# Kernel optimization log

Hardware: AMD Instinct MI355X
Metric: run time of the kernel (lower is better)

## Reference

```python
import jax, jax.numpy as jnp
import numpy as np

NEG = -1e30  # finite stand-in for -inf (keeps grads NaN-free)

T, B, V, L = 1024, 64, 128, 256


def setup_inputs() -> dict:
    key = jax.random.key(0)
    k1, k2 = jax.random.split(key)
    acts = jax.random.normal(k1, (T, B, V), dtype=jnp.float32)
    # flat concatenated labels, values in [1, V) (0 is the blank)
    labels = jax.random.randint(k2, (B * L,), 1, V, dtype=jnp.int32)
    act_lens = jnp.full((B,), T, dtype=jnp.int32)
    label_lens = jnp.full((B,), L, dtype=jnp.int32)
    return {"acts": acts, "labels": labels, "act_lens": act_lens, "label_lens": label_lens}


def _ctc_costs(acts, labels, act_lens, label_lens):
    # warp-ctc takes raw activations and applies softmax internally
    Tt, Bb, Vv = acts.shape
    Ll = labels.shape[0] // Bb
    blank = 0
    lab = labels.reshape(Bb, Ll)
    S = 2 * Ll + 1
    # extended label seq: blank, l1, blank, l2, ..., blank  -> (B, S)
    ext = jnp.full((Bb, S), blank, dtype=labels.dtype).at[:, 1::2].set(lab)
    # skip transition allowed where ext[s] != blank and ext[s] != ext[s-2]
    allow = jnp.concatenate(
        [jnp.zeros((Bb, 2), dtype=bool), (ext[:, 2:] != blank) & (ext[:, 2:] != ext[:, :-2])],
        axis=1,
    )
    log_probs = jax.nn.log_softmax(acts, axis=-1)  # (T, B, V)
    # emission log-probs along the extended label sequence: (T, B, S)
    emit_all = jnp.take_along_axis(log_probs, jnp.broadcast_to(ext[None], (Tt, Bb, S)), axis=2)

    alpha0 = (
        jnp.full((Bb, S), NEG, dtype=acts.dtype)
        .at[:, 0].set(emit_all[0, :, 0])
        .at[:, 1].set(emit_all[0, :, 1])
    )

    def step(alpha, xs):
        emit, t = xs  # emit: (B, S)
        p1 = jnp.pad(alpha[:, :-1], ((0, 0), (1, 0)), constant_values=NEG)
        p2 = jnp.pad(alpha[:, :-2], ((0, 0), (2, 0)), constant_values=NEG)
        p2 = jnp.where(allow, p2, NEG)
        m = jnp.maximum(jnp.maximum(alpha, p1), p2)
        new = m + jnp.log(jnp.exp(alpha - m) + jnp.exp(p1 - m) + jnp.exp(p2 - m)) + emit
        # freeze rows whose act_len is exhausted
        alpha = jnp.where((t < act_lens)[:, None], new, alpha)
        return alpha, None

    alphaT, _ = jax.lax.scan(step, alpha0, (emit_all[1:], jnp.arange(1, Tt)))
    end = (2 * label_lens).astype(jnp.int32)  # last blank position per example
    a_end = jnp.take_along_axis(alphaT, end[:, None], axis=1)[:, 0]
    a_end1 = jnp.take_along_axis(alphaT, (end - 1)[:, None], axis=1)[:, 0]
    return -jnp.logaddexp(a_end, a_end1)  # per-example negative log-likelihood


def reference(acts, labels, act_lens, label_lens):
    costs = _ctc_costs(acts, labels, act_lens, label_lens)
    return jnp.sum(costs)  # reduce=True, no size/length averaging
```

## Files before the change

### kernel.cpp

```cpp
#include <hip/hip_runtime.h>
#include <hip/hip_fp16.h>
#include <math.h>


#define L2E 1.4426950408889634f
#define LN2 0.6931471805599453f

constexpr int T   = 1024;
constexpr int B   = 64;
constexpr int V   = 128;
constexpr int L   = 256;
constexpr int RW  = 256;
constexpr int TP  = T + 32;

typedef float v2f __attribute__((ext_vector_type(2)));
typedef unsigned int v2u __attribute__((ext_vector_type(2)));

__device__ __forceinline__ v2f pk_fma(v2f a, v2f b, v2f c) {
  v2f d; asm("v_pk_fma_f32 %0, %1, %2, %3" : "=v"(d) : "v"(a), "v"(b), "v"(c));
  return d;
}
__device__ __forceinline__ v2f pk_mul(v2f a, v2f b) {
  v2f d; asm("v_pk_mul_f32 %0, %1, %2" : "=v"(d) : "v"(a), "v"(b)); return d;
}
__device__ __forceinline__ v2f pk_mul_s(v2f a, v2f sb) {
  v2f d; asm("v_pk_mul_f32 %0, %1, %2" : "=v"(d) : "v"(a), "s"(sb)); return d;
}
__device__ __forceinline__ v2f pk_fma_s(v2f a, v2f sb, v2f c) {
  v2f d; asm("v_pk_fma_f32 %0, %1, %2, %3" : "=v"(d) : "v"(a), "s"(sb), "v"(c));
  return d;
}

template <int CTRL>
__device__ __forceinline__ float fdpp0(float x) {
  return __int_as_float(__builtin_amdgcn_update_dpp(
      0, __float_as_int(x), CTRL, 0xf, 0xf, true));
}
template <int CTRL>
__device__ __forceinline__ float fdppk(float x) {
  return __int_as_float(__builtin_amdgcn_update_dpp(
      __float_as_int(x), __float_as_int(x), CTRL, 0xf, 0xf, false));
}

__device__ __forceinline__ float wave_bcast63(float x) {
  return __int_as_float(__builtin_amdgcn_readlane(__float_as_int(x), 63));
}

__device__ __forceinline__ float wave_max(float x) {
  x = fmaxf(x, fdppk<0x111>(x));
  x = fmaxf(x, fdppk<0x112>(x));
  x = fmaxf(x, fdppk<0x114>(x));
  x = fmaxf(x, fdppk<0x118>(x));
  x = fmaxf(x, fdppk<0x142>(x));
  x = fmaxf(x, fdppk<0x143>(x));
  return wave_bcast63(x);
}
__device__ __forceinline__ float wave_sum_nn(float x) {
  x += fdpp0<0x111>(x);
  x += fdpp0<0x112>(x);
  x += fdpp0<0x114>(x);
  x += fdpp0<0x118>(x);
  x += fdpp0<0x142>(x);
  x += fdpp0<0x143>(x);
  return wave_bcast63(x);
}

__device__ __forceinline__ float h2f(uint bits) {
  return __half2float(__ushort_as_half((ushort)bits));
}

__global__ __launch_bounds__(256) void ctc_probs_kernel(
    const float* __restrict__ acts,
    const int* __restrict__ labels,
    ushort* __restrict__ P,
    float* __restrict__ Pbk) {
  const int w    = threadIdx.x >> 6;
  const int lane = threadIdx.x & 63;
  const int b    = blockIdx.y;
  const int tb   = blockIdx.x * 32 + w * 8;

  if (tb >= T) {
    #pragma unroll
    for (int r = 0; r < 8; ++r) {
      uint2 z; z.x = 0u; z.y = 0u;
      *(uint2*)(P + ((size_t)b * TP + tb + r) * RW + 4 * lane) = z;
    }
    if (lane < 8) {
      v2f zp; zp.x = 0.f; zp.y = 0.f;
      *(v2f*)(Pbk + ((size_t)b * TP + tb + lane) * 2) = zp;
    }
    return;
  }

  const int4 lvv = *(const int4*)(labels + (size_t)b * L + 4 * lane);
  const int ba0 = (lvv.x & ~1) * 2, sh0 = (lvv.x & 1) << 4;
  const int ba1 = (lvv.y & ~1) * 2, sh1 = (lvv.y & 1) << 4;
  const int ba2 = (lvv.z & ~1) * 2, sh2 = (lvv.z & 1) << 4;
  const int ba3 = (lvv.w & ~1) * 2, sh3 = (lvv.w & 1) << 4;

  #pragma unroll
  for (int r = 0; r < 8; ++r) {
    const int t = tb + r;
    const float* row = acts + ((size_t)t * B + b) * V;
    const float2 v2 = *(const float2*)(row + 2 * lane);
    const float e0 = exp2f(fmaf(v2.x, L2E, -32.0f));
    const float e1 = exp2f(fmaf(v2.y, L2E, -32.0f));
    const float sm = wave_sum_nn(e0 + e1);
    const float rc = __builtin_amdgcn_rcpf(sm);
    const auto pk = __builtin_amdgcn_cvt_pkrtz(e0 * rc, e1 * rc);
    uint hp;
    __builtin_memcpy(&hp, &pk, 4);
    const uint g0 = (uint)__builtin_amdgcn_ds_bpermute(ba0, (int)hp);
    const uint g1 = (uint)__builtin_amdgcn_ds_bpermute(ba1, (int)hp);
    const uint g2 = (uint)__builtin_amdgcn_ds_bpermute(ba2, (int)hp);
    const uint g3 = (uint)__builtin_amdgcn_ds_bpermute(ba3, (int)hp);
    const uint h0 = (g0 >> sh0) & 0xffffu;
    const uint h1 = (g1 >> sh1) & 0xffffu;
    const uint h2 = (g2 >> sh2);
    const uint h3 = (g3 >> sh3);
    uint2 o;
    o.x = h0 | (h2 << 16);
    o.y = h1 | (h3 << 16);
    *(uint2*)(P + ((size_t)b * TP + t) * RW + 4 * lane) = o;
    if (lane == 0) {
      const float pb = e0 * rc;
      v2f bp; bp.x = pb; bp.y = pb;
      *(v2f*)(Pbk + ((size_t)b * TP + t) * 2) = bp;
    }
  }
}

__global__ __launch_bounds__(64) void ctc_dp_kernel(
    const ushort* __restrict__ P,
    const float* __restrict__ Pbk,
    const int* __restrict__ labels,
    const int* __restrict__ act_lens,
    const int* __restrict__ label_lens,
    float* __restrict__ out) {
  const int b    = blockIdx.x;
  const int lane = threadIdx.x;
  const ushort* __restrict__ Pb = P + (size_t)b * TP * RW;
  const float*  __restrict__ Bk = Pbk + (size_t)b * TP * 2;

  const int4 lv   = *(const int4*)(labels + (size_t)b * L + 4 * lane);
  const int prevw = __builtin_amdgcn_update_dpp(0, lv.w, 0x138, 0xf, 0xf, true);
  const float f0 = (lane > 0 && lv.x != 0 && lv.x != prevw) ? 1.f : 0.f;
  const float f1 = (lv.y != 0 && lv.y != lv.x) ? 1.f : 0.f;
  const float f2 = (lv.z != 0 && lv.z != lv.y) ? 1.f : 0.f;
  const float f3 = (lv.w != 0 && lv.w != lv.z) ? 1.f : 0.f;
  v2f F02; F02.x = f0; F02.y = f2;
  v2f F13; F13.x = f1; F13.y = f3;

  const int AL = act_lens[b];

  v2f P0, P1, P2, P3;
  P0.x=0.f; P0.y=0.f; P1.x=0.f; P1.y=0.f;
  P2.x=0.f; P2.y=0.f; P3.x=0.f; P3.y=0.f;
  float a8 = 0.f;
  {
    const uint2 u0 = *(const uint2*)(Pb + 4 * lane);
    const v2f bk0  = *(const v2f*)(Bk);
    const float eb0 = bk0.x;
    const float e00 = h2f(u0.x);
    if (lane == 0) { P0.x = eb0; P1.x = e00; }
  }
  int iacc = 0;
  float pend = 1.0f;

  auto step = [&](v2u u, v2f eb) {
    const float pc = fdpp0<0x138>(P3.y);
    v2f Q; Q.x = pc; Q.y = P3.x;
    v2f E02, E13;
    E02.x = h2f(u.x); E02.y = h2f(u.x >> 16);
    E13.x = h2f(u.y); E13.y = h2f(u.y >> 16);
    const v2f A1 = pk_fma(F02, Q, P0);
    const v2f A3 = pk_fma(F13, P1, P2);
    const v2f ZQ = pk_mul_s(Q, eb);
    const v2f Z2 = pk_mul_s(P1, eb);
    const v2f Z1 = pk_mul(A1, E02);
    const v2f Z3 = pk_mul(A3, E13);
    const float z8 = P3.y * eb.x;
    P0 = pk_fma_s(P0, eb, ZQ);
    P1 = pk_fma(P1, E02, Z1);
    P2 = pk_fma_s(P2, eb, Z2);
    P3 = pk_fma(P3, E13, Z3);
    a8 = fmaf(a8, eb.x, z8);
  };

  auto measure = [&]() {
    float m = fmaxf(fmaxf(fmaxf(P0.x, P0.y), fmaxf(P1.x, P1.y)),
                    fmaxf(fmaxf(P2.x, P2.y), fmaxf(P3.x, P3.y)));
    m = fmaxf(m, a8);
    pend = wave_max(m);
  };
  auto apply = [&]() {
    const uint mb = __float_as_uint(pend);
    int e = (int)((mb >> 23) & 0xffu); if (e < 48) e = 48;
    const float r = __uint_as_float((uint)(302 - e) << 23);
    iacc += (e - 175);
    v2f rr; rr.x = r; rr.y = r;
    P0 = pk_mul(P0, rr); P1 = pk_mul(P1, rr);
    P2 = pk_mul(P2, rr); P3 = pk_mul(P3, rr);
    a8 *= r;
  };

  uint2 evi[16];
  #pragma unroll
  for (int k = 0; k < 16; ++k)
    evi[k] = *(const uint2*)(Pb + (size_t)(1 + k) * RW + 4 * lane);
  v2f ebq[16];
  #pragma unroll
  for (int k = 0; k < 16; ++k)
    ebq[k] = *(const v2f*)(Bk + (size_t)(1 + k) * 2);

  const ushort* pf = Pb + (size_t)17 * RW;
  int t0 = 1;
  #pragma unroll 1
  for (int blk = 0; blk < 64; ++blk) {
    v2f ebn[16];
    {
      const float* bn = Bk + (size_t)(t0 + 16) * 2;
      #pragma unroll
      for (int k = 0; k < 16; ++k) ebn[k] = *(const v2f*)(bn + 2 * k);
    }
    const ushort* pfA = pf;
    const ushort* pfB = pf + (size_t)8 * RW;
    const bool fast = (t0 + 16 <= AL);
    if (fast) {
      #pragma unroll
      for (int k = 0; k < 16; ++k) {
        const uint2 uu = evi[k];
        v2u u; u.x = uu.x; u.y = uu.y;
        evi[k] = *(const uint2*)(((k < 8) ? pfA : pfB)
                                 + (size_t)(k & 7) * RW + 4 * lane);
        step(u, ebq[k]);
        if (k == 13) measure();
        if (k == 15) apply();
      }
    } else {
      #pragma unroll
      for (int k = 0; k < 16; ++k) {
        const uint2 uu = evi[k];
        v2u u; u.x = uu.x; u.y = uu.y;
        evi[k] = *(const uint2*)(((k < 8) ? pfA : pfB)
                                 + (size_t)(k & 7) * RW + 4 * lane);
        if ((t0 + k) < AL) step(u, ebq[k]);
        if (k == 13) measure();
        if (k == 15) apply();
      }
    }
    #pragma unroll
    for (int k = 0; k < 16; ++k) ebq[k] = ebn[k];
    t0 += 16;
    pf += (size_t)16 * RW;
  }

  const int end  = 2 * label_lens[b];
  const int base = 8 * lane;
  float sel = 0.f;
  if (base     == end || base     == end - 1) sel += P0.x;
  if (base + 1 == end || base + 1 == end - 1) sel += P1.x;
  if (base + 2 == end || base + 2 == end - 1) sel += P2.x;
  if (base + 3 == end || base + 3 == end - 1) sel += P3.x;
  if (base + 4 == end || base + 4 == end - 1) sel += P0.y;
  if (base + 5 == end || base + 5 == end - 1) sel += P1.y;
  if (base + 6 == end || base + 6 == end - 1) sel += P2.y;
  if (base + 7 == end || base + 7 == end - 1) sel += P3.y;
  if (lane == 63 && (end == 512 || end - 1 == 512)) sel += a8;
  sel = wave_sum_nn(sel);
  if (lane == 0) {
    const float cost = -((log2f(sel) + (float)iacc) * LN2);
    atomicAdd(out, cost);
  }
}

extern "C" void kernel_launch(void* const* d_in, const int* in_sizes, int n_in,
                              void* d_out, int out_size, void* d_ws, size_t ws_size,
                              hipStream_t stream) {
  const float* acts       = (const float*)d_in[0];
  const int*   labels     = (const int*)d_in[1];
  const int*   act_lens   = (const int*)d_in[2];
  const int*   label_lens = (const int*)d_in[3];
  float* out = (float*)d_out;
  ushort* P   = (ushort*)d_ws;
  float*  Pbk = (float*)(P + (size_t)B * TP * RW);

  (void)hipMemsetAsync(out, 0, sizeof(float) * out_size, stream);
  ctc_probs_kernel<<<dim3(TP / 32, B), 256, 0, stream>>>(acts, labels, P, Pbk);
  ctc_dp_kernel<<<B, 64, 0, stream>>>(P, Pbk, labels, act_lens, label_lens, out);
}
```

Baseline: 150.2 us.

## Split CTC alpha recursion across eight waves with overlapping halo lanes

The DP kernel moves from one wave per example, where each lane held 8 states, to 512 threads (8 waves) per example, with each lane holding 2 states. Waves overlap by 32 lanes as a halo, so each wave advances 16 timesteps on its own, then trades boundary state through shared memory and a block barrier. The scale max also becomes block-wide through shared memory. The probs kernel changes its fp16 packing order and stores the blank probability once instead of duplicated. This is meant to shorten the serial dependency chain per step, at the cost of redundant halo compute, a __syncthreads every 16 steps, and halo accuracy that relies on the 32-lane overlap covering 16 steps of propagation.

```diff
diff --git a/kernel.cpp b/kernel.cpp
--- a/kernel.cpp
+++ b/kernel.cpp
@@ -14,22 +14,6 @@
 constexpr int TP  = T + 32;
 
 typedef float v2f __attribute__((ext_vector_type(2)));
-typedef unsigned int v2u __attribute__((ext_vector_type(2)));
-
-__device__ __forceinline__ v2f pk_fma(v2f a, v2f b, v2f c) {
-  v2f d; asm("v_pk_fma_f32 %0, %1, %2, %3" : "=v"(d) : "v"(a), "v"(b), "v"(c));
-  return d;
-}
-__device__ __forceinline__ v2f pk_mul(v2f a, v2f b) {
-  v2f d; asm("v_pk_mul_f32 %0, %1, %2" : "=v"(d) : "v"(a), "v"(b)); return d;
-}
-__device__ __forceinline__ v2f pk_mul_s(v2f a, v2f sb) {
-  v2f d; asm("v_pk_mul_f32 %0, %1, %2" : "=v"(d) : "v"(a), "s"(sb)); return d;
-}
-__device__ __forceinline__ v2f pk_fma_s(v2f a, v2f sb, v2f c) {
-  v2f d; asm("v_pk_fma_f32 %0, %1, %2, %3" : "=v"(d) : "v"(a), "s"(sb), "v"(c));
-  return d;
-}
 
 template <int CTRL>
 __device__ __forceinline__ float fdpp0(float x) {
@@ -85,10 +69,7 @@
       uint2 z; z.x = 0u; z.y = 0u;
       *(uint2*)(P + ((size_t)b * TP + tb + r) * RW + 4 * lane) = z;
     }
-    if (lane < 8) {
-      v2f zp; zp.x = 0.f; zp.y = 0.f;
-      *(v2f*)(Pbk + ((size_t)b * TP + tb + lane) * 2) = zp;
-    }
+    if (lane < 8) Pbk[(size_t)b * TP + tb + lane] = 0.f;
     return;
   }
 
@@ -116,160 +97,158 @@
     const uint g3 = (uint)__builtin_amdgcn_ds_bpermute(ba3, (int)hp);
     const uint h0 = (g0 >> sh0) & 0xffffu;
     const uint h1 = (g1 >> sh1) & 0xffffu;
-    const uint h2 = (g2 >> sh2);
+    const uint h2 = (g2 >> sh2) & 0xffffu;
     const uint h3 = (g3 >> sh3);
     uint2 o;
-    o.x = h0 | (h2 << 16);
-    o.y = h1 | (h3 << 16);
+    o.x = h0 | (h1 << 16);
+    o.y = h2 | (h3 << 16);
     *(uint2*)(P + ((size_t)b * TP + t) * RW + 4 * lane) = o;
-    if (lane == 0) {
-      const float pb = e0 * rc;
-      v2f bp; bp.x = pb; bp.y = pb;
-      *(v2f*)(Pbk + ((size_t)b * TP + t) * 2) = bp;
-    }
-  }
-}
-
-__global__ __launch_bounds__(64) void ctc_dp_kernel(
+    if (lane == 0)
+      Pbk[(size_t)b * TP + t] = e0 * rc;
+  }
+}
+
+__global__ __launch_bounds__(512) void ctc_dp_kernel(
     const ushort* __restrict__ P,
     const float* __restrict__ Pbk,
     const int* __restrict__ labels,
     const int* __restrict__ act_lens,
     const int* __restrict__ label_lens,
     float* __restrict__ out) {
+  __shared__ float shc[2][9 * 64];
+  __shared__ float shm[2][8];
+  __shared__ float shs[8];
   const int b    = blockIdx.x;
-  const int lane = threadIdx.x;
+  const int w    = threadIdx.x >> 6;
+  const int lane = threadIdx.x & 63;
+  const int k    = 32 * w - 32 + lane;
+  const int kc   = (k < 0) ? 0 : k;
   const ushort* __restrict__ Pb = P + (size_t)b * TP * RW;
-  const float*  __restrict__ Bk = Pbk + (size_t)b * TP * 2;
-
-  const int4 lv   = *(const int4*)(labels + (size_t)b * L + 4 * lane);
-  const int prevw = __builtin_amdgcn_update_dpp(0, lv.w, 0x138, 0xf, 0xf, true);
-  const float f0 = (lane > 0 && lv.x != 0 && lv.x != prevw) ? 1.f : 0.f;
-  const float f1 = (lv.y != 0 && lv.y != lv.x) ? 1.f : 0.f;
-  const float f2 = (lv.z != 0 && lv.z != lv.y) ? 1.f : 0.f;
-  const float f3 = (lv.w != 0 && lv.w != lv.z) ? 1.f : 0.f;
-  v2f F02; F02.x = f0; F02.y = f2;
-  v2f F13; F13.x = f1; F13.y = f3;
+  const float*  __restrict__ Bk = Pbk + (size_t)b * TP;
+
+  if (threadIdx.x < 64) {
+    shc[0][threadIdx.x] = 0.f;
+    shc[1][threadIdx.x] = 0.f;
+  }
+
+  float f = 0.f;
+  if (k >= 1) {
+    const int la  = labels[(size_t)b * L + k];
+    const int lam = labels[(size_t)b * L + k - 1];
+    f = (la != 0 && la != lam) ? 1.f : 0.f;
+  }
 
   const int AL = act_lens[b];
-
-  v2f P0, P1, P2, P3;
-  P0.x=0.f; P0.y=0.f; P1.x=0.f; P1.y=0.f;
-  P2.x=0.f; P2.y=0.f; P3.x=0.f; P3.y=0.f;
+  const ushort* __restrict__ PbL = Pb + kc;
+
+  v2f Pp; Pp.x = 0.f; Pp.y = 0.f;
   float a8 = 0.f;
   {
-    const uint2 u0 = *(const uint2*)(Pb + 4 * lane);
-    const v2f bk0  = *(const v2f*)(Bk);
-    const float eb0 = bk0.x;
-    const float e00 = h2f(u0.x);
-    if (lane == 0) { P0.x = eb0; P1.x = e00; }
+    const float eb0 = Bk[0];
+    const float e00 = h2f(PbL[0]);
+    if (k == 0) { Pp.x = eb0; Pp.y = e00; }
   }
   int iacc = 0;
-  float pend = 1.0f;
-
-  auto step = [&](v2u u, v2f eb) {
-    const float pc = fdpp0<0x138>(P3.y);
-    v2f Q; Q.x = pc; Q.y = P3.x;
-    v2f E02, E13;
-    E02.x = h2f(u.x); E02.y = h2f(u.x >> 16);
-    E13.x = h2f(u.y); E13.y = h2f(u.y >> 16);
-    const v2f A1 = pk_fma(F02, Q, P0);
-    const v2f A3 = pk_fma(F13, P1, P2);
-    const v2f ZQ = pk_mul_s(Q, eb);
-    const v2f Z2 = pk_mul_s(P1, eb);
-    const v2f Z1 = pk_mul(A1, E02);
-    const v2f Z3 = pk_mul(A3, E13);
-    const float z8 = P3.y * eb.x;
-    P0 = pk_fma_s(P0, eb, ZQ);
-    P1 = pk_fma(P1, E02, Z1);
-    P2 = pk_fma_s(P2, eb, Z2);
-    P3 = pk_fma(P3, E13, Z3);
-    a8 = fmaf(a8, eb.x, z8);
-  };
-
-  auto measure = [&]() {
-    float m = fmaxf(fmaxf(fmaxf(P0.x, P0.y), fmaxf(P1.x, P1.y)),
-                    fmaxf(fmaxf(P2.x, P2.y), fmaxf(P3.x, P3.y)));
-    m = fmaxf(m, a8);
-    pend = wave_max(m);
-  };
-  auto apply = [&]() {
-    const uint mb = __float_as_uint(pend);
-    int e = (int)((mb >> 23) & 0xffu); if (e < 48) e = 48;
-    const float r = __uint_as_float((uint)(302 - e) << 23);
-    iacc += (e - 175);
-    v2f rr; rr.x = r; rr.y = r;
-    P0 = pk_mul(P0, rr); P1 = pk_mul(P1, rr);
-    P2 = pk_mul(P2, rr); P3 = pk_mul(P3, rr);
-    a8 *= r;
-  };
-
-  uint2 evi[16];
+
+  uint ev[16];
   #pragma unroll
-  for (int k = 0; k < 16; ++k)
-    evi[k] = *(const uint2*)(Pb + (size_t)(1 + k) * RW + 4 * lane);
-  v2f ebq[16];
+  for (int j = 0; j < 16; ++j) ev[j] = PbL[(size_t)(1 + j) * RW];
+  float bkq[16];
   #pragma unroll
-  for (int k = 0; k < 16; ++k)
-    ebq[k] = *(const v2f*)(Bk + (size_t)(1 + k) * 2);
-
-  const ushort* pf = Pb + (size_t)17 * RW;
+  for (int j = 0; j < 16; ++j) bkq[j] = Bk[1 + j];
+
+  const ushort* pf = PbL + (size_t)17 * RW;
   int t0 = 1;
   #pragma unroll 1
   for (int blk = 0; blk < 64; ++blk) {
-    v2f ebn[16];
+    const int bb = blk & 1;
+    float bkn[16];
     {
-      const float* bn = Bk + (size_t)(t0 + 16) * 2;
+      const float* bn = Bk + (t0 + 16);
       #pragma unroll
-      for (int k = 0; k < 16; ++k) ebn[k] = *(const v2f*)(bn + 2 * k);
+      for (int j = 0; j < 16; ++j) bkn[j] = bn[j];
     }
     const ushort* pfA = pf;
     const ushort* pfB = pf + (size_t)8 * RW;
     const bool fast = (t0 + 16 <= AL);
     if (fast) {
       #pragma unroll
-      for (int k = 0; k < 16; ++k) {
-        const uint2 uu = evi[k];
-        v2u u; u.x = uu.x; u.y = uu.y;
-        evi[k] = *(const uint2*)(((k < 8) ? pfA : pfB)
-                                 + (size_t)(k & 7) * RW + 4 * lane);
-        step(u, ebq[k]);
-        if (k == 13) measure();
-        if (k == 15) apply();
+      for (int kk = 0; kk < 16; ++kk) {
+        const uint uu = ev[kk];
+        ev[kk] = ((kk < 8) ? pfA : pfB)[(size_t)(kk & 7) * RW];
+        const float pc = fdpp0<0x138>(Pp.y);
+        const float e  = h2f(uu);
+        const float sx = Pp.x + pc;
+        const float ty = fmaf(f, pc, Pp.y + Pp.x);
+        const float s8 = a8 + Pp.y;
+        Pp.x = sx * bkq[kk];
+        Pp.y = ty * e;
+        a8 = s8 * bkq[kk];
+        if (kk == 13) {
+          const float m = fmaxf(fmaxf(Pp.x, Pp.y), a8);
+          const float pm = wave_max(m);
+          if (lane == 0) shm[bb][w] = pm;
+        }
       }
     } else {
       #pragma unroll
-      for (int k = 0; k < 16; ++k) {
-        const uint2 uu = evi[k];
-        v2u u; u.x = uu.x; u.y = uu.y;
-        evi[k] = *(const uint2*)(((k < 8) ? pfA : pfB)
-                                 + (size_t)(k & 7) * RW + 4 * lane);
-        if ((t0 + k) < AL) step(u, ebq[k]);
-        if (k == 13) measure();
-        if (k == 15) apply();
+      for (int kk = 0; kk < 16; ++kk) {
+        const uint uu = ev[kk];
+        ev[kk] = ((kk < 8) ? pfA : pfB)[(size_t)(kk & 7) * RW];
+        if ((t0 + kk) < AL) {
+          const float pc = fdpp0<0x138>(Pp.y);
+          const float e  = h2f(uu);
+          const float sx = Pp.x + pc;
+          const float ty = fmaf(f, pc, Pp.y + Pp.x);
+          const float s8 = a8 + Pp.y;
+          Pp.x = sx * bkq[kk];
+          Pp.y = ty * e;
+          a8 = s8 * bkq[kk];
+        }
+        if (kk == 13) {
+          const float m = fmaxf(fmaxf(Pp.x, Pp.y), a8);
+          const float pm = wave_max(m);
+          if (lane == 0) shm[bb][w] = pm;
+        }
       }
     }
+    if (lane >= 32)
+      *(v2f*)&shc[bb][(w + 1) * 64 + 2 * (lane - 32)] = Pp;
+    __syncthreads();
+    const float* mm = shm[bb];
+    const float bm = fmaxf(fmaxf(fmaxf(mm[0], mm[1]), fmaxf(mm[2], mm[3])),
+                           fmaxf(fmaxf(mm[4], mm[5]), fmaxf(mm[6], mm[7])));
+    if (lane < 32)
+      Pp = *(const v2f*)&shc[bb][w * 64 + 2 * lane];
+    {
+      const uint mb2 = __float_as_uint(bm);
+      int e = (int)((mb2 >> 23) & 0xffu); if (e < 48) e = 48;
+      const float r = __uint_as_float((uint)(302 - e) << 23);
+      iacc += (e - 175);
+      Pp.x *= r; Pp.y *= r; a8 *= r;
+    }
     #pragma unroll
-    for (int k = 0; k < 16; ++k) ebq[k] = ebn[k];
+    for (int j = 0; j < 16; ++j) bkq[j] = bkn[j];
     t0 += 16;
     pf += (size_t)16 * RW;
   }
 
-  const int end  = 2 * label_lens[b];
-  const int base = 8 * lane;
+  const int end = 2 * label_lens[b];
   float sel = 0.f;
-  if (base     == end || base     == end - 1) sel += P0.x;
-  if (base + 1 == end || base + 1 == end - 1) sel += P1.x;
-  if (base + 2 == end || base + 2 == end - 1) sel += P2.x;
-  if (base + 3 == end || base + 3 == end - 1) sel += P3.x;
-  if (base + 4 == end || base + 4 == end - 1) sel += P0.y;
-  if (base + 5 == end || base + 5 == end - 1) sel += P1.y;
-  if (base + 6 == end || base + 6 == end - 1) sel += P2.y;
-  if (base + 7 == end || base + 7 == end - 1) sel += P3.y;
-  if (lane == 63 && (end == 512 || end - 1 == 512)) sel += a8;
+  if (lane >= 32) {
+    const int c0 = 64 * w + 2 * (lane - 32);
+    if (c0 == end || c0 == end - 1) sel += Pp.x;
+    if (c0 + 1 == end || c0 + 1 == end - 1) sel += Pp.y;
+  }
+  if (w == 7 && lane == 63 && end == 512) sel += a8;
   sel = wave_sum_nn(sel);
-  if (lane == 0) {
-    const float cost = -((log2f(sel) + (float)iacc) * LN2);
+  if (lane == 0) shs[w] = sel;
+  __syncthreads();
+  if (threadIdx.x == 0) {
+    float s = 0.f;
+    #pragma unroll
+    for (int j = 0; j < 8; ++j) s += shs[j];
+    const float cost = -((log2f(s) + (float)iacc) * LN2);
     atomicAdd(out, cost);
   }
 }
@@ -287,5 +266,5 @@
 
   (void)hipMemsetAsync(out, 0, sizeof(float) * out_size, stream);
   ctc_probs_kernel<<<dim3(TP / 32, B), 256, 0, stream>>>(acts, labels, P, Pbk);
-  ctc_dp_kernel<<<B, 64, 0, stream>>>(P, Pbk, labels, act_lens, label_lens, out);
-}
+  ctc_dp_kernel<<<B, 512, 0, stream>>>(P, Pbk, labels, act_lens, label_lens, out);
+}
```

Result: faster. 142.9 us (-4.9%).

## Replace packed-FP32 DP step with scalar add-then-multiply inline asm

Applied to the files above, without the earlier changes.

The CTC alpha recurrence step moves from packed v_pk_fma/v_pk_mul on interleaved register pairs to a scalar form: add neighbours, fmac the skip term, then multiply by the emission, written as one hand-scheduled inline-asm block. The probability layout is changed to a natural contiguous half order, and the blank-probability buffer is stored as single floats instead of duplicated pairs, with its loads interleaved into the prefetch loop. The aim is a shorter serial dependency chain per timestep and fewer registers for prefetch buffers, at the cost of giving up packed throughput and fixing the schedule in asm volatile.

```diff
diff --git a/kernel.cpp b/kernel.cpp
--- a/kernel.cpp
+++ b/kernel.cpp
@@ -12,24 +12,6 @@
 constexpr int L   = 256;
 constexpr int RW  = 256;
 constexpr int TP  = T + 32;
-
-typedef float v2f __attribute__((ext_vector_type(2)));
-typedef unsigned int v2u __attribute__((ext_vector_type(2)));
-
-__device__ __forceinline__ v2f pk_fma(v2f a, v2f b, v2f c) {
-  v2f d; asm("v_pk_fma_f32 %0, %1, %2, %3" : "=v"(d) : "v"(a), "v"(b), "v"(c));
-  return d;
-}
-__device__ __forceinline__ v2f pk_mul(v2f a, v2f b) {
-  v2f d; asm("v_pk_mul_f32 %0, %1, %2" : "=v"(d) : "v"(a), "v"(b)); return d;
-}
-__device__ __forceinline__ v2f pk_mul_s(v2f a, v2f sb) {
-  v2f d; asm("v_pk_mul_f32 %0, %1, %2" : "=v"(d) : "v"(a), "s"(sb)); return d;
-}
-__device__ __forceinline__ v2f pk_fma_s(v2f a, v2f sb, v2f c) {
-  v2f d; asm("v_pk_fma_f32 %0, %1, %2, %3" : "=v"(d) : "v"(a), "s"(sb), "v"(c));
-  return d;
-}
 
 template <int CTRL>
 __device__ __forceinline__ float fdpp0(float x) {
@@ -67,6 +49,46 @@
 
 __device__ __forceinline__ float h2f(uint bits) {
   return __half2float(__ushort_as_half((ushort)bits));
+}
+
+__device__ __forceinline__ void step22(
+    float& a0, float& a1, float& a2, float& a3, float& a4,
+    float& a5, float& a6, float& a7, float& a8,
+    float pc, float e0, float e1, float e2, float e3, float eb,
+    float f0, float f1, float f2, float f3) {
+  float s0, s1, s2, s3, s4, s5, s6, s7, s8;
+  asm volatile(
+      "v_add_f32 %[s8], %[x8], %[x7]\n\t"
+      "v_add_f32 %[s7], %[x7], %[x6]\n\t"
+      "v_add_f32 %[s6], %[x6], %[x5]\n\t"
+      "v_add_f32 %[s5], %[x5], %[x4]\n\t"
+      "v_add_f32 %[s4], %[x4], %[x3]\n\t"
+      "v_add_f32 %[s3], %[x3], %[x2]\n\t"
+      "v_add_f32 %[s2], %[x2], %[x1]\n\t"
+      "v_add_f32 %[s1], %[x1], %[x0]\n\t"
+      "v_add_f32 %[s0], %[x0], %[pc]\n\t"
+      "v_fmac_f32 %[s7], %[f3], %[x5]\n\t"
+      "v_fmac_f32 %[s5], %[f2], %[x3]\n\t"
+      "v_fmac_f32 %[s3], %[f1], %[x1]\n\t"
+      "v_fmac_f32 %[s1], %[f0], %[pc]\n\t"
+      "v_mul_f32 %[x8], %[s8], %[eb]\n\t"
+      "v_mul_f32 %[x7], %[s7], %[e3]\n\t"
+      "v_mul_f32 %[x6], %[s6], %[eb]\n\t"
+      "v_mul_f32 %[x5], %[s5], %[e2]\n\t"
+      "v_mul_f32 %[x4], %[s4], %[eb]\n\t"
+      "v_mul_f32 %[x3], %[s3], %[e1]\n\t"
+      "v_mul_f32 %[x2], %[s2], %[eb]\n\t"
+      "v_mul_f32 %[x1], %[s1], %[e0]\n\t"
+      "v_mul_f32 %[x0], %[s0], %[eb]\n\t"
+      : [s0] "=&v"(s0), [s1] "=&v"(s1), [s2] "=&v"(s2), [s3] "=&v"(s3),
+        [s4] "=&v"(s4), [s5] "=&v"(s5), [s6] "=&v"(s6), [s7] "=&v"(s7),
+        [s8] "=&v"(s8),
+        [x0] "+v"(a0), [x1] "+v"(a1), [x2] "+v"(a2), [x3] "+v"(a3),
+        [x4] "+v"(a4), [x5] "+v"(a5), [x6] "+v"(a6), [x7] "+v"(a7),
+        [x8] "+v"(a8)
+      : [pc] "v"(pc), [e0] "v"(e0), [e1] "v"(e1), [e2] "v"(e2),
+        [e3] "v"(e3), [eb] "v"(eb), [f0] "v"(f0), [f1] "v"(f1),
+        [f2] "v"(f2), [f3] "v"(f3));
 }
 
 __global__ __launch_bounds__(256) void ctc_probs_kernel(
@@ -85,10 +107,7 @@
       uint2 z; z.x = 0u; z.y = 0u;
       *(uint2*)(P + ((size_t)b * TP + tb + r) * RW + 4 * lane) = z;
     }
-    if (lane < 8) {
-      v2f zp; zp.x = 0.f; zp.y = 0.f;
-      *(v2f*)(Pbk + ((size_t)b * TP + tb + lane) * 2) = zp;
-    }
+    if (lane < 8) Pbk[(size_t)b * TP + tb + lane] = 0.f;
     return;
   }
 
@@ -116,17 +135,14 @@
     const uint g3 = (uint)__builtin_amdgcn_ds_bpermute(ba3, (int)hp);
     const uint h0 = (g0 >> sh0) & 0xffffu;
     const uint h1 = (g1 >> sh1) & 0xffffu;
-    const uint h2 = (g2 >> sh2);
+    const uint h2 = (g2 >> sh2) & 0xffffu;
     const uint h3 = (g3 >> sh3);
     uint2 o;
-    o.x = h0 | (h2 << 16);
-    o.y = h1 | (h3 << 16);
+    o.x = h0 | (h1 << 16);
+    o.y = h2 | (h3 << 16);
     *(uint2*)(P + ((size_t)b * TP + t) * RW + 4 * lane) = o;
-    if (lane == 0) {
-      const float pb = e0 * rc;
-      v2f bp; bp.x = pb; bp.y = pb;
-      *(v2f*)(Pbk + ((size_t)b * TP + t) * 2) = bp;
-    }
+    if (lane == 0)
+      Pbk[(size_t)b * TP + t] = e0 * rc;
   }
 }
 
@@ -140,7 +156,7 @@
   const int b    = blockIdx.x;
   const int lane = threadIdx.x;
   const ushort* __restrict__ Pb = P + (size_t)b * TP * RW;
-  const float*  __restrict__ Bk = Pbk + (size_t)b * TP * 2;
+  const float*  __restrict__ Bk = Pbk + (size_t)b * TP;
 
   const int4 lv   = *(const int4*)(labels + (size_t)b * L + 4 * lane);
   const int prevw = __builtin_amdgcn_update_dpp(0, lv.w, 0x138, 0xf, 0xf, true);
@@ -148,48 +164,22 @@
   const float f1 = (lv.y != 0 && lv.y != lv.x) ? 1.f : 0.f;
   const float f2 = (lv.z != 0 && lv.z != lv.y) ? 1.f : 0.f;
   const float f3 = (lv.w != 0 && lv.w != lv.z) ? 1.f : 0.f;
-  v2f F02; F02.x = f0; F02.y = f2;
-  v2f F13; F13.x = f1; F13.y = f3;
 
   const int AL = act_lens[b];
 
-  v2f P0, P1, P2, P3;
-  P0.x=0.f; P0.y=0.f; P1.x=0.f; P1.y=0.f;
-  P2.x=0.f; P2.y=0.f; P3.x=0.f; P3.y=0.f;
-  float a8 = 0.f;
+  float a0=0.f,a1=0.f,a2=0.f,a3=0.f,a4=0.f,a5=0.f,a6=0.f,a7=0.f,a8=0.f;
   {
     const uint2 u0 = *(const uint2*)(Pb + 4 * lane);
-    const v2f bk0  = *(const v2f*)(Bk);
-    const float eb0 = bk0.x;
+    const float eb0 = Bk[0];
     const float e00 = h2f(u0.x);
-    if (lane == 0) { P0.x = eb0; P1.x = e00; }
+    if (lane == 0) { a0 = eb0; a1 = e00; }
   }
   int iacc = 0;
   float pend = 1.0f;
 
-  auto step = [&](v2u u, v2f eb) {
-    const float pc = fdpp0<0x138>(P3.y);
-    v2f Q; Q.x = pc; Q.y = P3.x;
-    v2f E02, E13;
-    E02.x = h2f(u.x); E02.y = h2f(u.x >> 16);
-    E13.x = h2f(u.y); E13.y = h2f(u.y >> 16);
-    const v2f A1 = pk_fma(F02, Q, P0);
-    const v2f A3 = pk_fma(F13, P1, P2);
-    const v2f ZQ = pk_mul_s(Q, eb);
-    const v2f Z2 = pk_mul_s(P1, eb);
-    const v2f Z1 = pk_mul(A1, E02);
-    const v2f Z3 = pk_mul(A3, E13);
-    const float z8 = P3.y * eb.x;
-    P0 = pk_fma_s(P0, eb, ZQ);
-    P1 = pk_fma(P1, E02, Z1);
-    P2 = pk_fma_s(P2, eb, Z2);
-    P3 = pk_fma(P3, E13, Z3);
-    a8 = fmaf(a8, eb.x, z8);
-  };
-
   auto measure = [&]() {
-    float m = fmaxf(fmaxf(fmaxf(P0.x, P0.y), fmaxf(P1.x, P1.y)),
-                    fmaxf(fmaxf(P2.x, P2.y), fmaxf(P3.x, P3.y)));
+    float m = fmaxf(fmaxf(fmaxf(a0, a1), fmaxf(a2, a3)),
+                    fmaxf(fmaxf(a4, a5), fmaxf(a6, a7)));
     m = fmaxf(m, a8);
     pend = wave_max(m);
   };
@@ -198,42 +188,40 @@
     int e = (int)((mb >> 23) & 0xffu); if (e < 48) e = 48;
     const float r = __uint_as_float((uint)(302 - e) << 23);
     iacc += (e - 175);
-    v2f rr; rr.x = r; rr.y = r;
-    P0 = pk_mul(P0, rr); P1 = pk_mul(P1, rr);
-    P2 = pk_mul(P2, rr); P3 = pk_mul(P3, rr);
-    a8 *= r;
+    a0*=r; a1*=r; a2*=r; a3*=r; a4*=r; a5*=r; a6*=r; a7*=r; a8*=r;
   };
 
   uint2 evi[16];
+  float ebs[16];
   #pragma unroll
-  for (int k = 0; k < 16; ++k)
+  for (int k = 0; k < 16; ++k) {
     evi[k] = *(const uint2*)(Pb + (size_t)(1 + k) * RW + 4 * lane);
-  v2f ebq[16];
-  #pragma unroll
-  for (int k = 0; k < 16; ++k)
-    ebq[k] = *(const v2f*)(Bk + (size_t)(1 + k) * 2);
+    ebs[k] = Bk[1 + k];
+  }
 
   const ushort* pf = Pb + (size_t)17 * RW;
   int t0 = 1;
   #pragma unroll 1
   for (int blk = 0; blk < 64; ++blk) {
-    v2f ebn[16];
-    {
-      const float* bn = Bk + (size_t)(t0 + 16) * 2;
-      #pragma unroll
-      for (int k = 0; k < 16; ++k) ebn[k] = *(const v2f*)(bn + 2 * k);
-    }
     const ushort* pfA = pf;
     const ushort* pfB = pf + (size_t)8 * RW;
+    const float*  bf  = Bk + (t0 + 16);
     const bool fast = (t0 + 16 <= AL);
     if (fast) {
       #pragma unroll
       for (int k = 0; k < 16; ++k) {
         const uint2 uu = evi[k];
-        v2u u; u.x = uu.x; u.y = uu.y;
+        const float ebv = ebs[k];
         evi[k] = *(const uint2*)(((k < 8) ? pfA : pfB)
                                  + (size_t)(k & 7) * RW + 4 * lane);
-        step(u, ebq[k]);
+        ebs[k] = bf[k];
+        const float pc = fdpp0<0x138>(a7);
+        const float e0 = h2f(uu.x);
+        const float e1 = h2f(uu.x >> 16);
+        const float e2 = h2f(uu.y);
+        const float e3 = h2f(uu.y >> 16);
+        step22(a0,a1,a2,a3,a4,a5,a6,a7,a8, pc, e0,e1,e2,e3, ebv,
+               f0,f1,f2,f3);
         if (k == 13) measure();
         if (k == 15) apply();
       }
@@ -241,16 +229,23 @@
       #pragma unroll
       for (int k = 0; k < 16; ++k) {
         const uint2 uu = evi[k];
-        v2u u; u.x = uu.x; u.y = uu.y;
+        const float ebv = ebs[k];
         evi[k] = *(const uint2*)(((k < 8) ? pfA : pfB)
                                  + (size_t)(k & 7) * RW + 4 * lane);
-        if ((t0 + k) < AL) step(u, ebq[k]);
+        ebs[k] = bf[k];
+        if ((t0 + k) < AL) {
+          const float pc = fdpp0<0x138>(a7);
+          const float e0 = h2f(uu.x);
+          const float e1 = h2f(uu.x >> 16);
+          const float e2 = h2f(uu.y);
+          const float e3 = h2f(uu.y >> 16);
+          step22(a0,a1,a2,a3,a4,a5,a6,a7,a8, pc, e0,e1,e2,e3, ebv,
+                 f0,f1,f2,f3);
+        }
         if (k == 13) measure();
         if (k == 15) apply();
       }
     }
-    #pragma unroll
-    for (int k = 0; k < 16; ++k) ebq[k] = ebn[k];
     t0 += 16;
     pf += (size_t)16 * RW;
   }
@@ -258,14 +253,14 @@
   const int end  = 2 * label_lens[b];
   const int base = 8 * lane;
   float sel = 0.f;
-  if (base     == end || base     == end - 1) sel += P0.x;
-  if (base + 1 == end || base + 1 == end - 1) sel += P1.x;
-  if (base + 2 == end || base + 2 == end - 1) sel += P2.x;
-  if (base + 3 == end || base + 3 == end - 1) sel += P3.x;
-  if (base + 4 == end || base + 4 == end - 1) sel += P0.y;
-  if (base + 5 == end || base + 5 == end - 1) sel += P1.y;
-  if (base + 6 == end || base + 6 == end - 1) sel += P2.y;
-  if (base + 7 == end || base + 7 == end - 1) sel += P3.y;
+  if (base     == end || base     == end - 1) sel += a0;
+  if (base + 1 == end || base + 1 == end - 1) sel += a1;
+  if (base + 2 == end || base + 2 == end - 1) sel += a2;
+  if (base + 3 == end || base + 3 == end - 1) sel += a3;
+  if (base + 4 == end || base + 4 == end - 1) sel += a4;
+  if (base + 5 == end || base + 5 == end - 1) sel += a5;
+  if (base + 6 == end || base + 6 == end - 1) sel += a6;
+  if (base + 7 == end || base + 7 == end - 1) sel += a7;
   if (lane == 63 && (end == 512 || end - 1 == 512)) sel += a8;
   sel = wave_sum_nn(sel);
   if (lane == 0) {
```

Measured after the change: 163.9 us. +9.2%, slower.
